# Performance work log

Hardware: AMD Instinct MI355X
Metric: run time of the kernel (lower is better)

## Reference

```python
import jax, jax.numpy as jnp
import numpy as np

UNITS = 512

def setup_inputs() -> dict:
    key = jax.random.key(0)
    ks = jax.random.split(key, 5)
    B, T, V = 64, 1024, 1024
    x = jax.random.normal(ks[0], (B, T, V), dtype=jnp.float32)
    A_r = jax.random.normal(ks[1], (B, B), dtype=jnp.float32) * 0.1
    A_i = jax.random.normal(ks[2], (B, B), dtype=jnp.float32) * 0.1
    B_r = jax.random.normal(ks[3], (B, B), dtype=jnp.float32) * 0.1
    B_i = jax.random.normal(ks[4], (B, B), dtype=jnp.float32) * 0.1
    return {"x": x, "A_r": A_r, "A_i": A_i, "B_r": B_r, "B_i": B_i}

def _forward(x, A_r, A_i, B_r, B_i):
    units = UNITS
    Bn, T, V = x.shape
    A = (A_r + 1j * A_i).astype(jnp.complex64)    # recurrent weight, (Bn, Bn)
    Bm = (B_r + 1j * B_i).astype(jnp.complex64)   # input weight, (Bn, Bn)
    maxseq = max(units, T // 2 + 1, V // 2 + 1)
    seqlen = (maxseq - 1) * 2
    fftnorm = jnp.asarray(seqlen, dtype=jnp.complex64)
    xi = jnp.transpose(x, (0, 2, 1))                       # (Bn, V, T)
    X = jnp.fft.rfft2(xi, s=(seqlen, seqlen))              # (Bn, seqlen, seqlen//2+1)
    X = (X / fftnorm)[:, :units, :]
    X = (X / fftnorm)[:, :, :units]
    X = jnp.transpose(X, (0, 2, 1)).astype(jnp.complex64)  # (Bn, time=units, feat=units)

    z_init = jnp.zeros((Bn, units), dtype=jnp.complex64)

    def step(z, x_t):
        # method_one with activation=None: zi = (A@z0 + B@x0)/2 on feature-0 column
        zi = (A @ z[:, :1] + Bm @ x_t[:, :1]) * 0.5        # (Bn, 1)
        z_new = jnp.concatenate([z[:, 1:], zi], axis=1)    # rolled shift-register state
        y = zi + z_new                                     # broadcast (Bn,1)+(Bn,units)
        return z_new, y

    _, ys = jax.lax.scan(step, z_init, jnp.transpose(X, (1, 0, 2)))  # ys: (time, Bn, units)
    cout = jnp.transpose(ys, (1, 0, 2))                    # (Bn, time, units)
    out_c = jnp.transpose(cout, (0, 2, 1)) * fftnorm       # (Bn, units, units) complex64
    return jnp.stack([out_c.real, out_c.imag], axis=-1).astype(jnp.float32)

def reference(x, A_r, A_i, B_r, B_i):
    return _forward(x, A_r, A_i, B_r, B_i)
```

## Files before the change

### kernel.cpp

```cpp
#include <hip/hip_runtime.h>

#define BN 64
#define TN 1024
#define VN 1024
#define UNITSN 512
#define TWO_PI 6.283185307179586476925286766559f

typedef __attribute__((ext_vector_type(4))) float f32x4;

__global__ void k_reduce_v(const float* __restrict__ x, float* __restrict__ s) {
    int row  = blockIdx.x * 4 + (threadIdx.x >> 6);
    int lane = threadIdx.x & 63;
    const f32x4* xr = reinterpret_cast<const f32x4*>(x) + (size_t)row * (VN / 4);
    float acc = 0.f;
#pragma unroll
    for (int i = 0; i < 4; ++i) {
        f32x4 v = __builtin_nontemporal_load(&xr[i * 64 + lane]);
        acc += (v.x + v.y) + (v.z + v.w);
    }
#pragma unroll
    for (int off = 32; off > 0; off >>= 1)
        acc += __shfl_down(acc, off, 64);
    if (lane == 0) s[row] = acc;
}

__global__ void k_dft(const float* __restrict__ s, float2* __restrict__ F) {
    int w    = (blockIdx.x * blockDim.x + threadIdx.x) >> 6;
    int lane = threadIdx.x & 63;
    int b    = w >> 9;
    int t    = w & 511;
    const float* sb = s + b * TN;

    int p  = (lane * t) & 1023;
    int st = (64 * t) & 1023;

    float ar = 0.f, ai = 0.f;
#pragma unroll
    for (int i = 0; i < 16; ++i) {
        float sv  = sb[lane + 64 * i];
        float ang = (float)p * (-TWO_PI / 1024.0f);
        float c   = __cosf(ang);
        float n   = __sinf(ang);
        ar = fmaf(sv, c, ar);
        ai = fmaf(sv, n, ai);
        p  = (p + st) & 1023;
    }
#pragma unroll
    for (int off = 32; off > 0; off >>= 1) {
        ar += __shfl_xor(ar, off, 64);
        ai += __shfl_xor(ai, off, 64);
    }
    if (lane == 0) F[b * UNITSN + t] = make_float2(ar, ai);
}

__global__ void k_matmul(const float* __restrict__ Br, const float* __restrict__ Bi,
                         const float2* __restrict__ F, float2* __restrict__ W) {
    int tid   = threadIdx.x;
    int lane  = tid & 63;
    int wv    = tid >> 6;
    int b     = blockIdx.x >> 3;
    int tbase = ((blockIdx.x & 7) * 4 + wv) * 16;
    int t     = tbase + (lane & 15);
    int seg   = lane >> 4;
    const float* brp = Br + b * 64 + seg * 16;
    const float* bip = Bi + b * 64 + seg * 16;
    float wr = 0.f, wi = 0.f;
#pragma unroll
    for (int i = 0; i < 16; ++i) {
        float br = brp[i];
        float bi = bip[i];
        float2 f = F[(seg * 16 + i) * UNITSN + t];
        wr = fmaf(br, f.x, wr); wr = fmaf(-bi, f.y, wr);
        wi = fmaf(br, f.y, wi); wi = fmaf(bi, f.x, wi);
    }
    wr += __shfl_xor(wr, 16, 64); wi += __shfl_xor(wi, 16, 64);
    wr += __shfl_xor(wr, 32, 64); wi += __shfl_xor(wi, 32, 64);
    if (seg == 0) {
        const float coef = 1.0f / 2048.0f;
        W[b * UNITSN + t] = make_float2(wr * coef, wi * coef);
    }
}

__global__ void k_expand(const float2* __restrict__ W, f32x4* __restrict__ out) {
    int idx = blockIdx.x * 256 + threadIdx.x;
    int t2 = (idx & 255) * 2;
    int j  = (idx >> 8) & 511;
    int b  = idx >> 17;
    const float2* Wb = W + b * UNITSN;
    const f32x4 w01 = *reinterpret_cast<const f32x4*>(Wb + t2);
    int k0 = t2 + j - 511;
    float2 z0 = (k0 >= 0)     ? Wb[k0]     : make_float2(0.f, 0.f);
    float2 z1 = (k0 + 1 >= 0) ? Wb[k0 + 1] : make_float2(0.f, 0.f);
    f32x4 o = {w01.x + z0.x, w01.y + z0.y, w01.z + z1.x, w01.w + z1.y};
    __builtin_nontemporal_store(o, &out[idx]);
}

extern "C" void kernel_launch(void* const* d_in, const int* in_sizes, int n_in,
                              void* d_out, int out_size, void* d_ws, size_t ws_size,
                              hipStream_t stream) {
    const float* x  = (const float*)d_in[0];
    const float* Br = (const float*)d_in[3];
    const float* Bi = (const float*)d_in[4];

    char* ws = (char*)d_ws;
    float*  s = (float*)ws;
    float2* F = (float2*)(ws + 256 * 1024);
    float2* W = (float2*)(ws + 512 * 1024);

    k_reduce_v<<<BN * TN / 4, 256, 0, stream>>>(x, s);
    k_dft<<<(BN * UNITSN) / 4, 256, 0, stream>>>(s, F);
    k_matmul<<<BN * 8, 256, 0, stream>>>(Br, Bi, F, W);
    k_expand<<<(BN * UNITSN * (UNITSN / 2)) / 256, 256, 0, stream>>>(W, (f32x4*)d_out);
}
```

Before: 79.69 us.

## Fuse B-matrix multiply into output expansion kernel using LDS

Merges the complex B@F matmul with the shift-register expansion into one kernel. Each block recomputes the 512-entry W row for its batch into shared memory, then writes 32 output rows from LDS. This removes a kernel launch and the global write and read of W. The cost is that the matmul work is redundantly recomputed 16 times per batch row, and the stores wait for that compute to finish.

```diff
diff --git a/kernel.cpp b/kernel.cpp
--- a/kernel.cpp
+++ b/kernel.cpp
@@ -53,46 +53,44 @@
     if (lane == 0) F[b * UNITSN + t] = make_float2(ar, ai);
 }
 
-__global__ void k_matmul(const float* __restrict__ Br, const float* __restrict__ Bi,
-                         const float2* __restrict__ F, float2* __restrict__ W) {
-    int tid   = threadIdx.x;
-    int lane  = tid & 63;
-    int wv    = tid >> 6;
-    int b     = blockIdx.x >> 3;
-    int tbase = ((blockIdx.x & 7) * 4 + wv) * 16;
-    int t     = tbase + (lane & 15);
-    int seg   = lane >> 4;
-    const float* brp = Br + b * 64 + seg * 16;
-    const float* bip = Bi + b * 64 + seg * 16;
-    float wr = 0.f, wi = 0.f;
-#pragma unroll
-    for (int i = 0; i < 16; ++i) {
-        float br = brp[i];
-        float bi = bip[i];
-        float2 f = F[(seg * 16 + i) * UNITSN + t];
-        wr = fmaf(br, f.x, wr); wr = fmaf(-bi, f.y, wr);
-        wi = fmaf(br, f.y, wi); wi = fmaf(bi, f.x, wi);
+__global__ void k_mm_expand(const float* __restrict__ Br, const float* __restrict__ Bi,
+                            const float2* __restrict__ F, f32x4* __restrict__ out) {
+    __shared__ float2 Wlds[UNITSN];
+    int tid = threadIdx.x;
+    int b   = blockIdx.x >> 4;
+    int jc  = blockIdx.x & 15;
+
+    const float* brp = Br + b * 64;
+    const float* bip = Bi + b * 64;
+    float wra = 0.f, wia = 0.f, wrb = 0.f, wib = 0.f;
+#pragma unroll 8
+    for (int k = 0; k < 64; ++k) {
+        float br = brp[k];
+        float bi = bip[k];
+        float2 fa = F[k * UNITSN + tid];
+        float2 fb = F[k * UNITSN + tid + 256];
+        wra = fmaf(br, fa.x, wra); wra = fmaf(-bi, fa.y, wra);
+        wia = fmaf(br, fa.y, wia); wia = fmaf(bi, fa.x, wia);
+        wrb = fmaf(br, fb.x, wrb); wrb = fmaf(-bi, fb.y, wrb);
+        wib = fmaf(br, fb.y, wib); wib = fmaf(bi, fb.x, wib);
     }
-    wr += __shfl_xor(wr, 16, 64); wi += __shfl_xor(wi, 16, 64);
-    wr += __shfl_xor(wr, 32, 64); wi += __shfl_xor(wi, 32, 64);
-    if (seg == 0) {
-        const float coef = 1.0f / 2048.0f;
-        W[b * UNITSN + t] = make_float2(wr * coef, wi * coef);
+    const float coef = 1.0f / 2048.0f;
+    Wlds[tid]       = make_float2(wra * coef, wia * coef);
+    Wlds[tid + 256] = make_float2(wrb * coef, wib * coef);
+    __syncthreads();
+
+    size_t outBase = ((size_t)b << 17) + ((size_t)jc << 13);
+#pragma unroll 4
+    for (int it = 0; it < 32; ++it) {
+        int j  = jc * 32 + it;
+        int t2 = tid * 2;
+        f32x4 w01 = *reinterpret_cast<const f32x4*>(&Wlds[t2]);
+        int k0 = t2 + j - 511;
+        float2 z0 = (k0 >= 0)     ? Wlds[k0]     : make_float2(0.f, 0.f);
+        float2 z1 = (k0 + 1 >= 0) ? Wlds[k0 + 1] : make_float2(0.f, 0.f);
+        f32x4 o = {w01.x + z0.x, w01.y + z0.y, w01.z + z1.x, w01.w + z1.y};
+        __builtin_nontemporal_store(o, &out[outBase + ((size_t)it << 8) + tid]);
     }
-}
-
-__global__ void k_expand(const float2* __restrict__ W, f32x4* __restrict__ out) {
-    int idx = blockIdx.x * 256 + threadIdx.x;
-    int t2 = (idx & 255) * 2;
-    int j  = (idx >> 8) & 511;
-    int b  = idx >> 17;
-    const float2* Wb = W + b * UNITSN;
-    const f32x4 w01 = *reinterpret_cast<const f32x4*>(Wb + t2);
-    int k0 = t2 + j - 511;
-    float2 z0 = (k0 >= 0)     ? Wb[k0]     : make_float2(0.f, 0.f);
-    float2 z1 = (k0 + 1 >= 0) ? Wb[k0 + 1] : make_float2(0.f, 0.f);
-    f32x4 o = {w01.x + z0.x, w01.y + z0.y, w01.z + z1.x, w01.w + z1.y};
-    __builtin_nontemporal_store(o, &out[idx]);
 }
 
 extern "C" void kernel_launch(void* const* d_in, const int* in_sizes, int n_in,
@@ -105,10 +103,8 @@
     char* ws = (char*)d_ws;
     float*  s = (float*)ws;
     float2* F = (float2*)(ws + 256 * 1024);
-    float2* W = (float2*)(ws + 512 * 1024);
 
     k_reduce_v<<<BN * TN / 4, 256, 0, stream>>>(x, s);
     k_dft<<<(BN * UNITSN) / 4, 256, 0, stream>>>(s, F);
-    k_matmul<<<BN * 8, 256, 0, stream>>>(Br, Bi, F, W);
-    k_expand<<<(BN * UNITSN * (UNITSN / 2)) / 256, 256, 0, stream>>>(W, (f32x4*)d_out);
+    k_mm_expand<<<BN * 16, 256, 0, stream>>>(Br, Bi, F, (f32x4*)d_out);
 }
```

New measurement: 84.98 us. 6.6% more time.
